# Kernel tuning notes

Measured on AMD Instinct MI355X. Metric: run time of the kernel, lower is better.

The kernel has to match this reference:

```python
import jax, jax.numpy as jnp
import numpy as np
import math

N_HEADS = 4
GELU = lambda x: jax.nn.gelu(x, approximate=False)  # torch nn.GELU default = exact erf

def _ln(x, s, b):
    m = jnp.mean(x, axis=-1, keepdims=True)
    v = jnp.mean((x - m) ** 2, axis=-1, keepdims=True)
    return (x - m) * jax.lax.rsqrt(v + 1e-5) * s + b

def _fwd(materials, in_seq, proj_vars, param_vars, enc_w1, enc_b1, enc_w2, enc_b2, sos,
         tl_wq, tl_wk, tl_wv, tl_bq, tl_bk, tl_bv, tl_wo, tl_bo,
         tl_ln1s, tl_ln1b, tl_ln2s, tl_ln2b, tl_fw1, tl_fb1, tl_fw2, tl_fb2,
         pw1, pb1, pw2, pb2, pw3, pb3, pw4, pb4, pw5, pb5,
         ipw1, ipb1, ipw2, ipb2, hw1, hb1, hw2, hb2, hw3, hb3):
    B = in_seq.shape[0]
    # encoder input MLP: [B,S,1] -> [B,S,D]
    x = GELU(in_seq @ enc_w1 + enc_b1) @ enc_w2 + enc_b2
    x = jnp.concatenate([jnp.broadcast_to(sos, (B, 1, sos.shape[-1])), x], axis=1)
    S1, D = x.shape[1], x.shape[2]
    dh = D // N_HEADS
    # sinusoidal positional encoding
    pos = jnp.arange(S1, dtype=jnp.float32)[:, None]
    div = jnp.exp(jnp.arange(0, D, 2, dtype=jnp.float32) * (-math.log(10000.0) / D))
    ang = pos * div
    pe = jnp.stack([jnp.sin(ang), jnp.cos(ang)], axis=-1).reshape(S1, D)
    x = x + pe
    scale = 1.0 / math.sqrt(dh)
    # post-LN TransformerEncoder layers (torch default norm_first=False), eval mode (no dropout)
    for l in range(tl_wq.shape[0]):
        q = (x @ tl_wq[l] + tl_bq[l]).reshape(B, S1, N_HEADS, dh).transpose(0, 2, 1, 3)
        k = (x @ tl_wk[l] + tl_bk[l]).reshape(B, S1, N_HEADS, dh).transpose(0, 2, 1, 3)
        v = (x @ tl_wv[l] + tl_bv[l]).reshape(B, S1, N_HEADS, dh).transpose(0, 2, 1, 3)
        att = jax.nn.softmax(jnp.einsum('bhqd,bhkd->bhqk', q, k) * scale, axis=-1)
        o = jnp.einsum('bhqk,bhkd->bhqd', att, v).transpose(0, 2, 1, 3).reshape(B, S1, D)
        x = _ln(x + o @ tl_wo[l] + tl_bo[l], tl_ln1s[l], tl_ln1b[l])
        f = GELU(x @ tl_fw1[l] + tl_fb1[l]) @ tl_fw2[l] + tl_fb2[l]
        x = _ln(x + f, tl_ln2s[l], tl_ln2b[l])
    sos_out = x[:, 0]
    h = jnp.concatenate([proj_vars, sos_out], axis=1)
    for w, b in ((pw1, pb1), (pw2, pb2), (pw3, pb3), (pw4, pb4)):
        h = GELU(h @ w + b)
    proj_out = h @ pw5 + pb5
    pp = GELU(param_vars @ ipw1 + ipb1) @ ipw2 + ipb2
    mi = jnp.concatenate([pp, proj_out], axis=1)  # [B, output_features+param_vars]
    # MaterialHead mask-gather-MLP-scatter == run every tiny head densely, pick by material id
    h1 = GELU(jnp.einsum('bi,mio->mbo', mi, hw1) + hb1[:, None, :])
    h2 = GELU(jnp.einsum('mbi,mio->mbo', h1, hw2) + hb2[:, None, :])
    h3 = jnp.einsum('mbi,mio->mbo', h2, hw3) + hb3[:, None, :]  # [M,B,1]
    return h3[materials, jnp.arange(B)]  # [B,1]

def setup_inputs() -> dict:
    key = jax.random.key(0)
    ks = iter(jax.random.split(key, 64))
    def rn(shape, scale=0.05):
        return jax.random.normal(next(ks), shape, dtype=jnp.float32) * scale
    B, S, IN, EL, D, L, DFF = 64, 1024, 1, 48, 64, 3, 256
    PV, PP, OF, M = 3, 3, 24, 3
    IF = OF + PP
    return dict(
        in_seq=rn((B, S, IN), 1.0),
        proj_vars=rn((B, PV), 1.0),
        param_vars=rn((B, PP), 1.0),
        materials=jax.random.randint(next(ks), (B,), 0, M),
        enc_w1=rn((IN, EL)), enc_b1=rn((EL,)), enc_w2=rn((EL, D)), enc_b2=rn((D,)),
        sos=rn((1, 1, D)),
        tl_wq=rn((L, D, D)), tl_wk=rn((L, D, D)), tl_wv=rn((L, D, D)),
        tl_bq=rn((L, D)), tl_bk=rn((L, D)), tl_bv=rn((L, D)),
        tl_wo=rn((L, D, D)), tl_bo=rn((L, D)),
        tl_ln1s=jnp.ones((L, D)), tl_ln1b=jnp.zeros((L, D)),
        tl_ln2s=jnp.ones((L, D)), tl_ln2b=jnp.zeros((L, D)),
        tl_fw1=rn((L, D, DFF)), tl_fb1=rn((L, DFF)), tl_fw2=rn((L, DFF, D)), tl_fb2=rn((L, D)),
        pw1=rn((PV + D, 34)), pb1=rn((34,)), pw2=rn((34, 11)), pb2=rn((11,)),
        pw3=rn((11, 36)), pb3=rn((36,)), pw4=rn((36, 22)), pb4=rn((22,)),
        pw5=rn((22, OF)), pb5=rn((OF,)),
        ipw1=rn((PP, 3)), ipb1=rn((3,)), ipw2=rn((3, PP)), ipb2=rn((PP,)),
        hw1=rn((M, IF, 15)), hb1=rn((M, 15)), hw2=rn((M, 15, 18)), hb2=rn((M, 18)),
        hw3=rn((M, 18, 1)), hb3=rn((M, 1)),
    )

def reference(in_seq, proj_vars, param_vars, materials, enc_w1, enc_b1, enc_w2, enc_b2, sos,
              tl_wq, tl_wk, tl_wv, tl_bq, tl_bk, tl_bv, tl_wo, tl_bo,
              tl_ln1s, tl_ln1b, tl_ln2s, tl_ln2b, tl_fw1, tl_fb1, tl_fw2, tl_fb2,
              pw1, pb1, pw2, pb2, pw3, pb3, pw4, pb4, pw5, pb5,
              ipw1, ipb1, ipw2, ipb2, hw1, hb1, hw2, hb2, hw3, hb3):
    return _fwd(materials, in_seq, proj_vars, param_vars, enc_w1, enc_b1, enc_w2, enc_b2, sos,
                tl_wq, tl_wk, tl_wv, tl_bq, tl_bk, tl_bv, tl_wo, tl_bo,
                tl_ln1s, tl_ln1b, tl_ln2s, tl_ln2b, tl_fw1, tl_fb1, tl_fw2, tl_fb2,
                pw1, pb1, pw2, pb2, pw3, pb3, pw4, pb4, pw5, pb5,
                ipw1, ipb1, ipw2, ipb2, hw1, hb1, hw2, hb2, hw3, hb3)
```

## Files before the change

kernel.cpp:

```cpp
#include <hip/hip_runtime.h>
#include <hip/hip_bf16.h>
#include <math.h>

#define BB   64
#define SS   1024
#define S1C  1025
#define DD   64
#define NHD  4
#define NBH  (BB * NHD)
#define DHD  16
#define DFFC 256
#define NLAY 3
#define NTOK (BB * S1C)
#define SPAD 1056
#define TGRP 11
#define FTQ   32
#define FT2   32
#define OPAD 68
#define QSCL 0.36067376022224085f

typedef const float* fp;
typedef __attribute__((ext_vector_type(8))) short bf16x8;
typedef __attribute__((ext_vector_type(4))) float f32x4;
typedef __attribute__((ext_vector_type(2))) unsigned int u32x2;
typedef __attribute__((ext_vector_type(4))) unsigned int u32x4;

#if __has_builtin(__builtin_amdgcn_exp2f)
#define RAW_EXP2(x) __builtin_amdgcn_exp2f(x)
#else
#define RAW_EXP2(x) __expf(0.6931471805599453f * (x))
#endif
#if __has_builtin(__builtin_amdgcn_rcpf)
#define RAW_RCP(x) __builtin_amdgcn_rcpf(x)
#else
#define RAW_RCP(x) (1.0f / (x))
#endif

__device__ __forceinline__ float gelu_exact(float x) {
    return 0.5f * x * (1.0f + erff(x * 0.7071067811865475f));
}
__device__ __forceinline__ float erf_fast(float x) {
    float ax = fabsf(x);
    float t = RAW_RCP(1.0f + 0.3275911f * ax);
    float p = t * (0.254829592f + t * (-0.284496736f + t * (1.421413741f +
              t * (-1.453152027f + t * 1.061405429f))));
    float e = RAW_EXP2(ax * ax * -1.4426950408889634f);
    float r = 1.0f - p * e;
    return copysignf(r, x);
}
__device__ __forceinline__ float gelu_fast(float x) {
    return 0.5f * x * (1.0f + erf_fast(x * 0.7071067811865475f));
}
__device__ __forceinline__ short f2b(float f) {
    unsigned u = __float_as_uint(f);
    return (short)((u + 0x7fffu + ((u >> 16) & 1u)) >> 16);
}

__device__ __forceinline__ u32x2 pack4exp(f32x4 c, bool valid) {
    float e0 = valid ? RAW_EXP2(c[0]) : 0.f;
    float e1 = valid ? RAW_EXP2(c[1]) : 0.f;
    float e2 = valid ? RAW_EXP2(c[2]) : 0.f;
    float e3 = valid ? RAW_EXP2(c[3]) : 0.f;
    unsigned r0, r1;
    asm("v_cvt_pk_bf16_f32 %0, %1, %2" : "=v"(r0) : "v"(e0), "v"(e1));
    asm("v_cvt_pk_bf16_f32 %0, %1, %2" : "=v"(r1) : "v"(e2), "v"(e3));
    return (u32x2){r0, r1};
}
__device__ __forceinline__ u32x2 pack4cvt(float x0, float x1, float x2, float x3) {
    unsigned r0, r1;
    asm("v_cvt_pk_bf16_f32 %0, %1, %2" : "=v"(r0) : "v"(x0), "v"(x1));
    asm("v_cvt_pk_bf16_f32 %0, %1, %2" : "=v"(r1) : "v"(x2), "v"(x3));
    return (u32x2){r0, r1};
}

__global__ __launch_bounds__(256) void k_wconv(
    fp wq, fp wk, fp wv, fp wo, fp w1, fp w2,
    short* __restrict__ wqkvT, short* __restrict__ woT,
    short* __restrict__ w1T, short* __restrict__ w2T)
{
    int l = blockIdx.y;
    int i = blockIdx.x * 256 + threadIdx.x;
    if (i < 12288) {
        int p = i >> 12, rem = i & 4095;
        int d = rem >> 6, j = rem & 63;
        fp src = (p == 0 ? wq : p == 1 ? wk : wv) + (size_t)l * 4096;
        float v = src[j * 64 + d];
        if (p == 0) v *= QSCL;
        wqkvT[(size_t)l * 12288 + i] = f2b(v);
    } else if (i < 16384) {
        int rem = i - 12288;
        woT[(size_t)l * 4096 + rem] = f2b(wo[(size_t)l * 4096 + (rem & 63) * 64 + (rem >> 6)]);
    } else if (i < 32768) {
        int rem = i - 16384;
        w1T[(size_t)l * 16384 + rem] = f2b(w1[(size_t)l * 16384 + (rem & 63) * 256 + (rem >> 6)]);
    } else {
        int rem = i - 32768;
        w2T[(size_t)l * 16384 + rem] = f2b(w2[(size_t)l * 16384 + (rem & 255) * 64 + (rem >> 8)]);
    }
}

__global__ __launch_bounds__(64) void k_zero(
    short* __restrict__ qb, short* __restrict__ kb, short* __restrict__ vbt)
{
    int bh = blockIdx.x, t = threadIdx.x;
    for (int i = t; i < 31 * 16; i += 64) {
        int r = i >> 4, c = i & 15;
        size_t idx = ((size_t)bh * SPAD + 1025 + r) * 16 + c;
        qb[idx] = 0; kb[idx] = 0;
    }
    for (int i = t; i < 16 * 31; i += 64) {
        int e = i / 31, c = i % 31;
        vbt[((size_t)bh * 16 + e) * SPAD + 1025 + c] = 0;
    }
}

__global__ __launch_bounds__(256) void k_encqkv(
    fp in_seq, fp enc_w1, fp enc_b1, fp enc_w2, fp enc_b2, fp sos,
    const short* __restrict__ wqkvT, fp bq, fp bk, fp bv,
    float* __restrict__ x,
    short* __restrict__ qb, short* __restrict__ kb, short* __restrict__ vbt)
{
    int t = threadIdx.x;
    int tok0 = blockIdx.x * FTQ;
    int w = t >> 6, d = t & 63;
    __shared__ float e[4][48];
    __shared__ short xs[FTQ][72];

    int i2 = (d >> 1) * 2;
    float factor = RAW_EXP2((float)i2 * (-9.210340371976184f / 64.0f) * 1.4426950408889634f);
    for (int i = 0; i < 8; ++i) {
        int tl = i * 4 + w;
        int tok = tok0 + tl;
        int b = tok / S1C, s = tok % S1C;
        float val;
        if (s == 0) {
            val = sos[d];
        } else {
            float tin = in_seq[b * SS + (s - 1)];
            if (d < 48) e[w][d] = gelu_fast(tin * enc_w1[d] + enc_b1[d]);
            float acc = enc_b2[d];
            for (int j = 0; j < 48; ++j) acc += e[w][j] * enc_w2[j * DD + d];
            val = acc;
        }
        float ang = (float)s * factor;
        val += (d & 1) ? __cosf(ang) : __sinf(ang);
        x[(size_t)tok * DD + d] = val;
        xs[tl][d] = f2b(val);
    }
    __syncthreads();

    int l = t & 63;
    int quad = l >> 4, lo = l & 15;
    bf16x8 a0 = *(const bf16x8*)&xs[lo][quad * 8];
    bf16x8 a1 = *(const bf16x8*)&xs[lo][32 + quad * 8];
    bf16x8 a2 = *(const bf16x8*)&xs[16 + lo][quad * 8];
    bf16x8 a3 = *(const bf16x8*)&xs[16 + lo][32 + quad * 8];

    int n = w * 16 + lo;
    #pragma unroll
    for (int p = 0; p < 3; ++p) {
        const short* wT = wqkvT + (size_t)p * 4096 + (size_t)n * 64;
        bf16x8 b0 = *(const bf16x8*)(wT + quad * 8);
        bf16x8 b1 = *(const bf16x8*)(wT + 32 + quad * 8);
        f32x4 c0 = __builtin_amdgcn_mfma_f32_16x16x32_bf16(a0, b0, (f32x4){0,0,0,0}, 0, 0, 0);
        c0 = __builtin_amdgcn_mfma_f32_16x16x32_bf16(a1, b1, c0, 0, 0, 0);
        f32x4 c1 = __builtin_amdgcn_mfma_f32_16x16x32_bf16(a2, b0, (f32x4){0,0,0,0}, 0, 0, 0);
        c1 = __builtin_amdgcn_mfma_f32_16x16x32_bf16(a3, b1, c1, 0, 0, 0);
        float bias = (p == 0) ? bq[n] * QSCL : (p == 1) ? bk[n] : bv[n];
        #pragma unroll
        for (int r = 0; r < 4; ++r) {
            int tok = tok0 + quad * 4 + r;
            int bb0 = tok / S1C, ss0 = tok % S1C;
            int bh = bb0 * NHD + w;
            short val = f2b(c0[r] + bias);
            int tok2 = tok + 16;
            int bb1 = tok2 / S1C, ss1 = tok2 % S1C;
            int bh2 = bb1 * NHD + w;
            short val2 = f2b(c1[r] + bias);
            if (p == 0) {
                qb[((size_t)bh * SPAD + ss0) * 16 + lo] = val;
                qb[((size_t)bh2 * SPAD + ss1) * 16 + lo] = val2;
            } else if (p == 1) {
                kb[((size_t)bh * SPAD + ss0) * 16 + lo] = val;
                kb[((size_t)bh2 * SPAD + ss1) * 16 + lo] = val2;
            } else {
                vbt[((size_t)bh * 16 + lo) * SPAD + ss0] = val;
                vbt[((size_t)bh2 * 16 + lo) * SPAD + ss1] = val2;
            }
        }
    }
}

__global__ __launch_bounds__(128) void k_attn(
    const short* __restrict__ qb, const short* __restrict__ kb,
    const short* __restrict__ vbt, short* __restrict__ ob)
{
    int bid = blockIdx.x;
    int bh  = bid % NBH;
    int grp = bid / NBH;
    int b = bh >> 2, h = bh & 3;
    int t = threadIdx.x;
    int w = t >> 6, l = t & 63;
    int quad = l >> 4, lo = l & 15;
    int t0 = grp * 2 + w;
    int t1 = t0 + 22;
    int t2 = t0 + 44;
    int qg0 = t0 * 16, qg1 = t1 * 16, qg2 = t2 * 16;

    __shared__ u32x2 ptmem[2][408];
    char* ptc = (char*)&ptmem[w][0];
    unsigned ptbase = (unsigned)(uintptr_t)ptc;

    const short* qbase = qb + (size_t)bh * SPAD * 16;
    const short* kbase = kb + (size_t)bh * SPAD * 16;
    const short* vbase = vbt + (size_t)bh * 16 * SPAD;

    bf16x8 aQ0 = {0,0,0,0,0,0,0,0}, aQ1 = {0,0,0,0,0,0,0,0}, aQ2 = {0,0,0,0,0,0,0,0};
    if (quad < 2) {
        aQ0 = *(const bf16x8*)(qbase + ((size_t)(qg0 + lo)) * 16 + quad * 8);
        aQ1 = *(const bf16x8*)(qbase + ((size_t)(qg1 + lo)) * 16 + quad * 8);
        aQ2 = *(const bf16x8*)(qbase + ((size_t)(qg2 + lo)) * 16 + quad * 8);
    }

    const short ONE = 0x3F80;
    bf16x8 aOne = {ONE, ONE, ONE, ONE, ONE, ONE, ONE, ONE};

    f32x4 oc0 = {0.f,0.f,0.f,0.f}, oc1 = {0.f,0.f,0.f,0.f}, oc2 = {0.f,0.f,0.f,0.f};
    f32x4 dn0 = {0.f,0.f,0.f,0.f}, dn1 = {0.f,0.f,0.f,0.f}, dn2 = {0.f,0.f,0.f,0.f};

    unsigned wo0 = (unsigned)((lo >> 2) * 136 + (lo & 3) * 32 + quad * 8);
    unsigned ro = (unsigned)(quad * 272 + lo * 8);
    unsigned rdp = ptbase + ro;
    char* wbp = ptc + wo0;

    bf16x8 kxA, kyA, kxB, kyB, vA, vB;

    {
        const short* k0p = kbase + (size_t)lo * 16 + (quad & 1) * 8;
        kxA = *(const bf16x8*)k0p;
        kyA = *(const bf16x8*)(k0p + 256);
        vA  = *(const bf16x8*)(vbase + (size_t)lo * SPAD + quad * 8);
        const short* k1p = kbase + (size_t)(32 + lo) * 16 + (quad & 1) * 8;
        kxB = *(const bf16x8*)k1p;
        kyB = *(const bf16x8*)(k1p + 256);

        f32x4 c0 = __builtin_amdgcn_mfma_f32_16x16x32_bf16(aQ0, kxA, (f32x4){0.f,0.f,0.f,0.f}, 0, 0, 0);
        f32x4 c1 = __builtin_amdgcn_mfma_f32_16x16x32_bf16(aQ1, kxA, (f32x4){0.f,0.f,0.f,0.f}, 0, 0, 0);
        f32x4 c2 = __builtin_amdgcn_mfma_f32_16x16x32_bf16(aQ2, kxA, (f32x4){0.f,0.f,0.f,0.f}, 0, 0, 0);
        *(u32x2*)(wbp)        = pack4exp(c0, true);
        *(u32x2*)(wbp + 1088) = pack4exp(c1, true);
        *(u32x2*)(wbp + 2176) = pack4exp(c2, true);
        c0 = __builtin_amdgcn_mfma_f32_16x16x32_bf16(aQ0, kyA, (f32x4){0.f,0.f,0.f,0.f}, 0, 0, 0);
        c1 = __builtin_amdgcn_mfma_f32_16x16x32_bf16(aQ1, kyA, (f32x4){0.f,0.f,0.f,0.f}, 0, 0, 0);
        c2 = __builtin_amdgcn_mfma_f32_16x16x32_bf16(aQ2, kyA, (f32x4){0.f,0.f,0.f,0.f}, 0, 0, 0);
        *(u32x2*)(wbp + 544)  = pack4exp(c0, true);
        *(u32x2*)(wbp + 1632) = pack4exp(c1, true);
        *(u32x2*)(wbp + 2720) = pack4exp(c2, true);
    }

#define STEP(CH, TAIL, KXC, KYC, KXN, KYN, VP, VC) do {                       \
    int ch_ = (CH);                                                            \
    if (!(TAIL)) {                                                             \
        const short* kn_ = kbase + (size_t)((ch_ + 1) * 32 + lo) * 16 + (quad & 1) * 8; \
        KXN = *(const bf16x8*)kn_;                                             \
        KYN = *(const bf16x8*)(kn_ + 256);                                     \
    }                                                                          \
    VC = *(const bf16x8*)(vbase + (size_t)lo * SPAD + ch_ * 32 + quad * 8);    \
    u32x2 p00_, p01_, p10_, p11_, p20_, p21_;                                  \
    asm volatile("ds_read_b64_tr_b16 %0, %1"             : "=v"(p00_) : "v"(rdp) : "memory"); \
    asm volatile("ds_read_b64_tr_b16 %0, %1 offset:136"  : "=v"(p01_) : "v"(rdp) : "memory"); \
    asm volatile("ds_read_b64_tr_b16 %0, %1 offset:1088" : "=v"(p10_) : "v"(rdp) : "memory"); \
    asm volatile("ds_read_b64_tr_b16 %0, %1 offset:1224" : "=v"(p11_) : "v"(rdp) : "memory"); \
    asm volatile("ds_read_b64_tr_b16 %0, %1 offset:2176" : "=v"(p20_) : "v"(rdp) : "memory"); \
    asm volatile("ds_read_b64_tr_b16 %0, %1 offset:2312" : "=v"(p21_) : "v"(rdp) : "memory"); \
    u32x2 wt0x_, wt1x_, wt2x_, wt0y_, wt1y_, wt2y_;                            \
    {                                                                          \
        f32x4 c0_ = __builtin_amdgcn_mfma_f32_16x16x32_bf16(aQ0, KXC, (f32x4){0.f,0.f,0.f,0.f}, 0, 0, 0); \
        f32x4 c1_ = __builtin_amdgcn_mfma_f32_16x16x32_bf16(aQ1, KXC, (f32x4){0.f,0.f,0.f,0.f}, 0, 0, 0); \
        f32x4 c2_ = __builtin_amdgcn_mfma_f32_16x16x32_bf16(aQ2, KXC, (f32x4){0.f,0.f,0.f,0.f}, 0, 0, 0); \
        bool v0_ = !(TAIL) || (lo == 0);                                       \
        wt0x_ = pack4exp(c0_, v0_);                                            \
        wt1x_ = pack4exp(c1_, v0_);                                            \
        wt2x_ = pack4exp(c2_, v0_);                                            \
        c0_ = __builtin_amdgcn_mfma_f32_16x16x32_bf16(aQ0, KYC, (f32x4){0.f,0.f,0.f,0.f}, 0, 0, 0); \
        c1_ = __builtin_amdgcn_mfma_f32_16x16x32_bf16(aQ1, KYC, (f32x4){0.f,0.f,0.f,0.f}, 0, 0, 0); \
        c2_ = __builtin_amdgcn_mfma_f32_16x16x32_bf16(aQ2, KYC, (f32x4){0.f,0.f,0.f,0.f}, 0, 0, 0); \
        bool v1_ = !(TAIL);                                                    \
        wt0y_ = pack4exp(c0_, v1_);                                            \
        wt1y_ = pack4exp(c1_, v1_);                                            \
        wt2y_ = pack4exp(c2_, v1_);                                            \
    }                                                                          \
    asm volatile("s_waitcnt lgkmcnt(0)" ::: "memory");                         \
    __builtin_amdgcn_sched_barrier(0);                                         \
    u32x4 q0_; q0_[0] = p00_[0]; q0_[1] = p00_[1]; q0_[2] = p01_[0]; q0_[3] = p01_[1]; \
    u32x4 q1_; q1_[0] = p10_[0]; q1_[1] = p10_[1]; q1_[2] = p11_[0]; q1_[3] = p11_[1]; \
    u32x4 q2_; q2_[0] = p20_[0]; q2_[1] = p20_[1]; q2_[2] = p21_[0]; q2_[3] = p21_[1]; \
    bf16x8 pB0_ = __builtin_bit_cast(bf16x8, q0_);                             \
    bf16x8 pB1_ = __builtin_bit_cast(bf16x8, q1_);                             \
    bf16x8 pB2_ = __builtin_bit_cast(bf16x8, q2_);                             \
    oc0 = __builtin_amdgcn_mfma_f32_16x16x32_bf16(VP, pB0_, oc0, 0, 0, 0);     \
    dn0 = __builtin_amdgcn_mfma_f32_16x16x32_bf16(aOne, pB0_, dn0, 0, 0, 0);   \
    oc1 = __builtin_amdgcn_mfma_f32_16x16x32_bf16(VP, pB1_, oc1, 0, 0, 0);     \
    dn1 = __builtin_amdgcn_mfma_f32_16x16x32_bf16(aOne, pB1_, dn1, 0, 0, 0);   \
    oc2 = __builtin_amdgcn_mfma_f32_16x16x32_bf16(VP, pB2_, oc2, 0, 0, 0);     \
    dn2 = __builtin_amdgcn_mfma_f32_16x16x32_bf16(aOne, pB2_, dn2, 0, 0, 0);   \
    *(u32x2*)(wbp)        = wt0x_;                                             \
    *(u32x2*)(wbp + 544)  = wt0y_;                                             \
    *(u32x2*)(wbp + 1088) = wt1x_;                                             \
    *(u32x2*)(wbp + 1632) = wt1y_;                                             \
    *(u32x2*)(wbp + 2176) = wt2x_;                                             \
    *(u32x2*)(wbp + 2720) = wt2y_;                                             \
} while (0)

    for (int chp = 1; chp < 31; chp += 2) {
        STEP(chp,     0, kxA, kyA, kxB, kyB, vA, vB);
        STEP(chp + 1, 0, kxB, kyB, kxA, kyA, vB, vA);
    }
    STEP(31, 0, kxA, kyA, kxB, kyB, vA, vB);
    STEP(32, 1, kxB, kyB, kxA, kyA, vB, vA);
#undef STEP

    {
        u32x2 p00, p01, p10, p11, p20, p21;
        asm volatile("ds_read_b64_tr_b16 %0, %1"             : "=v"(p00) : "v"(rdp) : "memory");
        asm volatile("ds_read_b64_tr_b16 %0, %1 offset:136"  : "=v"(p01) : "v"(rdp) : "memory");
        asm volatile("ds_read_b64_tr_b16 %0, %1 offset:1088" : "=v"(p10) : "v"(rdp) : "memory");
        asm volatile("ds_read_b64_tr_b16 %0, %1 offset:1224" : "=v"(p11) : "v"(rdp) : "memory");
        asm volatile("ds_read_b64_tr_b16 %0, %1 offset:2176" : "=v"(p20) : "v"(rdp) : "memory");
        asm volatile("ds_read_b64_tr_b16 %0, %1 offset:2312" : "=v"(p21) : "v"(rdp) : "memory");
        asm volatile("s_waitcnt lgkmcnt(0)" ::: "memory");
        __builtin_amdgcn_sched_barrier(0);
        u32x4 q0; q0[0] = p00[0]; q0[1] = p00[1]; q0[2] = p01[0]; q0[3] = p01[1];
        u32x4 q1; q1[0] = p10[0]; q1[1] = p10[1]; q1[2] = p11[0]; q1[3] = p11[1];
        u32x4 q2; q2[0] = p20[0]; q2[1] = p20[1]; q2[2] = p21[0]; q2[3] = p21[1];
        bf16x8 pB0 = __builtin_bit_cast(bf16x8, q0);
        bf16x8 pB1 = __builtin_bit_cast(bf16x8, q1);
        bf16x8 pB2 = __builtin_bit_cast(bf16x8, q2);
        oc0 = __builtin_amdgcn_mfma_f32_16x16x32_bf16(vA, pB0, oc0, 0, 0, 0);
        dn0 = __builtin_amdgcn_mfma_f32_16x16x32_bf16(aOne, pB0, dn0, 0, 0, 0);
        oc1 = __builtin_amdgcn_mfma_f32_16x16x32_bf16(vA, pB1, oc1, 0, 0, 0);
        dn1 = __builtin_amdgcn_mfma_f32_16x16x32_bf16(aOne, pB1, dn1, 0, 0, 0);
        oc2 = __builtin_amdgcn_mfma_f32_16x16x32_bf16(vA, pB2, oc2, 0, 0, 0);
        dn2 = __builtin_amdgcn_mfma_f32_16x16x32_bf16(aOne, pB2, dn2, 0, 0, 0);
    }

    {
        int qrow = qg0 + lo;
        if (qrow < S1C) {
            float inv = 1.0f / dn0[0];
            unsigned p0 = (unsigned short)f2b(oc0[0] * inv) | ((unsigned)(unsigned short)f2b(oc0[1] * inv) << 16);
            unsigned p1 = (unsigned short)f2b(oc0[2] * inv) | ((unsigned)(unsigned short)f2b(oc0[3] * inv) << 16);
            *(uint2*)(ob + ((size_t)b * S1C + qrow) * DD + h * DHD + quad * 4) = make_uint2(p0, p1);
        }
    }
    {
        int qrow = qg1 + lo;
        if (qrow < S1C) {
            float inv = 1.0f / dn1[0];
            unsigned p0 = (unsigned short)f2b(oc1[0] * inv) | ((unsigned)(unsigned short)f2b(oc1[1] * inv) << 16);
            unsigned p1 = (unsigned short)f2b(oc1[2] * inv) | ((unsigned)(unsigned short)f2b(oc1[3] * inv) << 16);
            *(uint2*)(ob + ((size_t)b * S1C + qrow) * DD + h * DHD + quad * 4) = make_uint2(p0, p1);
        }
    }
    {
        int qrow = qg2 + lo;
        if (qrow < S1C) {
            float inv = 1.0f / dn2[0];
            unsigned p0 = (unsigned short)f2b(oc2[0] * inv) | ((unsigned)(unsigned short)f2b(oc2[1] * inv) << 16);
            unsigned p1 = (unsigned short)f2b(oc2[2] * inv) | ((unsigned)(unsigned short)f2b(oc2[3] * inv) << 16);
            *(uint2*)(ob + ((size_t)b * S1C + qrow) * DD + h * DHD + quad * 4) = make_uint2(p0, p1);
        }
    }
}

__global__ __launch_bounds__(256) void k_block(
    const short* __restrict__ ob, float* __restrict__ x,
    const short* __restrict__ woT, fp bo, fp ln1s, fp ln1b,
    const short* __restrict__ w1T, fp b1, const short* __restrict__ w2T, fp b2,
    fp ln2s, fp ln2b,
    const short* __restrict__ wqkvTn, fp bqn, fp bkn, fp bvn,
    short* __restrict__ qb, short* __restrict__ kb, short* __restrict__ vbt,
    int has_next)
{
    int blk = blockIdx.x, t = threadIdx.x;
    int tok0 = blk * FT2;
    int w = t >> 6, l = t & 63;
    int quad = l >> 4, lo = l & 15;

    __shared__ float otf[FT2][OPAD];
    __shared__ u32x2 hidtr[2][8][136];
    short* ysb = (short*)&otf[0][0];
    char*  hidc = (char*)&hidtr[0][0][0];
    unsigned hidbase = (unsigned)(uintptr_t)hidc;

    int tt8 = t >> 3;
    int d8s = (t & 7) * 8;
    const float* xrow = x + (size_t)(tok0 + tt8) * DD + d8s;
    float4 xpa = *(const float4*)xrow;
    float4 xpb = *(const float4*)(xrow + 4);
    float4 s1a = *(const float4*)(ln1s + d8s);
    float4 s1b = *(const float4*)(ln1s + d8s + 4);
    float4 b1a = *(const float4*)(ln1b + d8s);
    float4 b1b = *(const float4*)(ln1b + d8s + 4);

    {
        const short* obp0 = ob + ((size_t)(tok0 + lo)) * DD;
        const short* obp1 = ob + ((size_t)(tok0 + 16 + lo)) * DD;
        bf16x8 a0 = *(const bf16x8*)(obp0 + quad * 8);
        bf16x8 a1 = *(const bf16x8*)(obp0 + 32 + quad * 8);
        bf16x8 a2 = *(const bf16x8*)(obp1 + quad * 8);
        bf16x8 a3 = *(const bf16x8*)(obp1 + 32 + quad * 8);
        int n = w * 16 + lo;
        const short* wT = woT + (size_t)n * 64;
        bf16x8 b0 = *(const bf16x8*)(wT + quad * 8);
        bf16x8 bb = *(const bf16x8*)(wT + 32 + quad * 8);
        f32x4 c0 = __builtin_amdgcn_mfma_f32_16x16x32_bf16(a0, b0, (f32x4){0,0,0,0}, 0, 0, 0);
        c0 = __builtin_amdgcn_mfma_f32_16x16x32_bf16(a1, bb, c0, 0, 0, 0);
        f32x4 c1 = __builtin_amdgcn_mfma_f32_16x16x32_bf16(a2, b0, (f32x4){0,0,0,0}, 0, 0, 0);
        c1 = __builtin_amdgcn_mfma_f32_16x16x32_bf16(a3, bb, c1, 0, 0, 0);
        float bov = bo[n];
        #pragma unroll
        for (int r = 0; r < 4; ++r) {
            otf[quad * 4 + r][n] = c0[r] + bov;
            otf[16 + quad * 4 + r][n] = c1[r] + bov;
        }
    }
    __syncthreads();

    float yv[8];
    {
        float4 o0 = *(const float4*)&otf[tt8][d8s];
        float4 o1 = *(const float4*)&otf[tt8][d8s + 4];
        float v0 = o0.x + xpa.x, v1 = o0.y + xpa.y, v2 = o0.z + xpa.z, v3 = o0.w + xpa.w;
        float v4 = o1.x + xpb.x, v5 = o1.y + xpb.y, v6 = o1.z + xpb.z, v7 = o1.w + xpb.w;
        float sum = ((v0 + v1) + (v2 + v3)) + ((v4 + v5) + (v6 + v7));
        float vs = v0 * v0;
        vs = fmaf(v1, v1, vs); vs = fmaf(v2, v2, vs); vs = fmaf(v3, v3, vs);
        vs = fmaf(v4, v4, vs); vs = fmaf(v5, v5, vs); vs = fmaf(v6, v6, vs);
        vs = fmaf(v7, v7, vs);
        sum += __shfl_xor(sum, 1, 64); sum += __shfl_xor(sum, 2, 64); sum += __shfl_xor(sum, 4, 64);
        vs  += __shfl_xor(vs , 1, 64); vs  += __shfl_xor(vs , 2, 64); vs  += __shfl_xor(vs , 4, 64);
        float mean = sum * (1.0f / 64.0f);
        float var = vs * (1.0f / 64.0f) - mean * mean;
        float rs = rsqrtf(var + 1e-5f);
        yv[0] = (v0 - mean) * rs * s1a.x + b1a.x;
        yv[1] = (v1 - mean) * rs * s1a.y + b1a.y;
        yv[2] = (v2 - mean) * rs * s1a.z + b1a.z;
        yv[3] = (v3 - mean) * rs * s1a.w + b1a.w;
        yv[4] = (v4 - mean) * rs * s1b.x + b1b.x;
        yv[5] = (v5 - mean) * rs * s1b.y + b1b.y;
        yv[6] = (v6 - mean) * rs * s1b.z + b1b.z;
        yv[7] = (v7 - mean) * rs * s1b.w + b1b.w;
        u32x2 pa = pack4cvt(yv[0], yv[1], yv[2], yv[3]);
        u32x2 pb = pack4cvt(yv[4], yv[5], yv[6], yv[7]);
        *(u32x4*)&ysb[tt8 * 136 + d8s] = (u32x4){pa[0], pa[1], pb[0], pb[1]};
    }
    __syncthreads();

    {
        bf16x8 a0 = *(const bf16x8*)&ysb[(size_t)lo * 136 + quad * 8];
        bf16x8 a1 = *(const bf16x8*)&ysb[(size_t)lo * 136 + 32 + quad * 8];
        bf16x8 a2 = *(const bf16x8*)&ysb[(size_t)(16 + lo) * 136 + quad * 8];
        bf16x8 a3 = *(const bf16x8*)&ysb[(size_t)(16 + lo) * 136 + 32 + quad * 8];
        unsigned hoff = (unsigned)(w * 2176 + (lo >> 2) * 136 + (lo & 3) * 32 + quad * 8);
        #pragma unroll
        for (int i = 0; i < 4; ++i) {
            int n = w * 64 + i * 16 + lo;
            const short* wT = w1T + (size_t)n * 64;
            bf16x8 b0 = *(const bf16x8*)(wT + quad * 8);
            bf16x8 bb = *(const bf16x8*)(wT + 32 + quad * 8);
            f32x4 c0 = __builtin_amdgcn_mfma_f32_16x16x32_bf16(a0, b0, (f32x4){0,0,0,0}, 0, 0, 0);
            c0 = __builtin_amdgcn_mfma_f32_16x16x32_bf16(a1, bb, c0, 0, 0, 0);
            f32x4 c1 = __builtin_amdgcn_mfma_f32_16x16x32_bf16(a2, b0, (f32x4){0,0,0,0}, 0, 0, 0);
            c1 = __builtin_amdgcn_mfma_f32_16x16x32_bf16(a3, bb, c1, 0, 0, 0);
            float b1v = b1[n];
            unsigned off = hoff + (i >> 1) * 1088 + (i & 1) * 544;
            *(u32x2*)(hidc + off) = pack4cvt(
                gelu_fast(c0[0] + b1v), gelu_fast(c0[1] + b1v),
                gelu_fast(c0[2] + b1v), gelu_fast(c0[3] + b1v));
            *(u32x2*)(hidc + 8704 + off) = pack4cvt(
                gelu_fast(c1[0] + b1v), gelu_fast(c1[1] + b1v),
                gelu_fast(c1[2] + b1v), gelu_fast(c1[3] + b1v));
        }
    }
    __syncthreads();

    {
        f32x4 c20 = {0.f,0.f,0.f,0.f}, c21 = {0.f,0.f,0.f,0.f};
        const short* wT2 = w2T + (size_t)(w * 16 + lo) * 256;
        unsigned ro = (unsigned)(quad * 272 + lo * 8);
        unsigned tb0 = hidbase + ro;
        unsigned tb1 = hidbase + 8704 + ro;
        u32x2 pA0, pA1, pA2, pA3, pB0, pB1, pB2, pB3;

#define TRRD(dst, addr, OFFSTR) \
    asm volatile("ds_read_b64_tr_b16 %0, %1 offset:" OFFSTR : "=v"(dst) : "v"(addr))
#define ISS(P0,P1,P2,P3, O1, O2) \
    TRRD(P0, tb0, O1); TRRD(P1, tb0, O2); TRRD(P2, tb1, O1); TRRD(P3, tb1, O2)
#define W4 asm volatile("s_waitcnt lgkmcnt(4)" ::: "memory"); __builtin_amdgcn_sched_barrier(0)
#define W0 asm volatile("s_waitcnt lgkmcnt(0)" ::: "memory"); __builtin_amdgcn_sched_barrier(0)
#define CONS(P0,P1,P2,P3, BF) do { \
    u32x4 q0_; q0_[0]=P0[0]; q0_[1]=P0[1]; q0_[2]=P1[0]; q0_[3]=P1[1]; \
    u32x4 q1_; q1_[0]=P2[0]; q1_[1]=P2[1]; q1_[2]=P3[0]; q1_[3]=P3[1]; \
    c20 = __builtin_amdgcn_mfma_f32_16x16x32_bf16(__builtin_bit_cast(bf16x8,q0_), BF, c20, 0,0,0); \
    c21 = __builtin_amdgcn_mfma_f32_16x16x32_bf16(__builtin_bit_cast(bf16x8,q1_), BF, c21, 0,0,0); \
} while (0)

        bf16x8 bfA = *(const bf16x8*)(wT2 + quad * 8);
        ISS(pA0,pA1,pA2,pA3, "0",    "136");
        bf16x8 bfB = *(const bf16x8*)(wT2 + 32 + quad * 8);
        ISS(pB0,pB1,pB2,pB3, "1088", "1224");
        W4; CONS(pA0,pA1,pA2,pA3, bfA);
        bfA = *(const bf16x8*)(wT2 + 64 + quad * 8);
        ISS(pA0,pA1,pA2,pA3, "2176", "2312");
        W4; CONS(pB0,pB1,pB2,pB3, bfB);
        bfB = *(const bf16x8*)(wT2 + 96 + quad * 8);
        ISS(pB0,pB1,pB2,pB3, "3264", "3400");
        W4; CONS(pA0,pA1,pA2,pA3, bfA);
        bfA = *(const bf16x8*)(wT2 + 128 + quad * 8);
        ISS(pA0,pA1,pA2,pA3, "4352", "4488");
        W4; CONS(pB0,pB1,pB2,pB3, bfB);
        bfB = *(const bf16x8*)(wT2 + 160 + quad * 8);
        ISS(pB0,pB1,pB2,pB3, "5440", "5576");
        W4; CONS(pA0,pA1,pA2,pA3, bfA);
        bfA = *(const bf16x8*)(wT2 + 192 + quad * 8);
        ISS(pA0,pA1,pA2,pA3, "6528", "6664");
        W4; CONS(pB0,pB1,pB2,pB3, bfB);
        bfB = *(const bf16x8*)(wT2 + 224 + quad * 8);
        ISS(pB0,pB1,pB2,pB3, "7616", "7752");
        W4; CONS(pA0,pA1,pA2,pA3, bfA);
        W0; CONS(pB0,pB1,pB2,pB3, bfB);
#undef TRRD
#undef ISS
#undef W4
#undef W0
#undef CONS

        float b2v = b2[w * 16 + lo];
        #pragma unroll
        for (int r = 0; r < 4; ++r) {
            otf[quad * 4 + r][w * 16 + lo] = c20[r] + b2v;
            otf[16 + quad * 4 + r][w * 16 + lo] = c21[r] + b2v;
        }
    }
    __syncthreads();

    {
        float4 s2a = *(const float4*)(ln2s + d8s);
        float4 s2b = *(const float4*)(ln2s + d8s + 4);
        float4 b2a = *(const float4*)(ln2b + d8s);
        float4 b2b = *(const float4*)(ln2b + d8s + 4);
        float4 o0 = *(const float4*)&otf[tt8][d8s];
        float4 o1 = *(const float4*)&otf[tt8][d8s + 4];
        float v0 = o0.x + yv[0], v1 = o0.y + yv[1], v2 = o0.z + yv[2], v3 = o0.w + yv[3];
        float v4 = o1.x + yv[4], v5 = o1.y + yv[5], v6 = o1.z + yv[6], v7 = o1.w + yv[7];
        float sum = ((v0 + v1) + (v2 + v3)) + ((v4 + v5) + (v6 + v7));
        float vs = v0 * v0;
        vs = fmaf(v1, v1, vs); vs = fmaf(v2, v2, vs); vs = fmaf(v3, v3, vs);
        vs = fmaf(v4, v4, vs); vs = fmaf(v5, v5, vs); vs = fmaf(v6, v6, vs);
        vs = fmaf(v7, v7, vs);
        sum += __shfl_xor(sum, 1, 64); sum += __shfl_xor(sum, 2, 64); sum += __shfl_xor(sum, 4, 64);
        vs  += __shfl_xor(vs , 1, 64); vs  += __shfl_xor(vs , 2, 64); vs  += __shfl_xor(vs , 4, 64);
        float mean = sum * (1.0f / 64.0f);
        float var = vs * (1.0f / 64.0f) - mean * mean;
        float rs = rsqrtf(var + 1e-5f);
        float y0 = (v0 - mean) * rs * s2a.x + b2a.x;
        float y1 = (v1 - mean) * rs * s2a.y + b2a.y;
        float y2 = (v2 - mean) * rs * s2a.z + b2a.z;
        float y3 = (v3 - mean) * rs * s2a.w + b2a.w;
        float y4 = (v4 - mean) * rs * s2b.x + b2b.x;
        float y5 = (v5 - mean) * rs * s2b.y + b2b.y;
        float y6 = (v6 - mean) * rs * s2b.z + b2b.z;
        float y7 = (v7 - mean) * rs * s2b.w + b2b.w;
        float* xo = x + (size_t)(tok0 + tt8) * DD + d8s;
        *(float4*)xo = make_float4(y0, y1, y2, y3);
        *(float4*)(xo + 4) = make_float4(y4, y5, y6, y7);
        u32x2 pa = pack4cvt(y0, y1, y2, y3);
        u32x2 pb = pack4cvt(y4, y5, y6, y7);
        *(u32x4*)&ysb[tt8 * 136 + d8s] = (u32x4){pa[0], pa[1], pb[0], pb[1]};
    }
    __syncthreads();

    if (has_next) {
        bf16x8 a0 = *(const bf16x8*)&ysb[(size_t)lo * 136 + quad * 8];
        bf16x8 a1 = *(const bf16x8*)&ysb[(size_t)lo * 136 + 32 + quad * 8];
        bf16x8 a2 = *(const bf16x8*)&ysb[(size_t)(16 + lo) * 136 + quad * 8];
        bf16x8 a3 = *(const bf16x8*)&ysb[(size_t)(16 + lo) * 136 + 32 + quad * 8];
        int n = w * 16 + lo;
        #pragma unroll
        for (int p = 0; p < 3; ++p) {
            const short* wT = wqkvTn + (size_t)p * 4096 + (size_t)n * 64;
            bf16x8 b0 = *(const bf16x8*)(wT + quad * 8);
            bf16x8 bb = *(const bf16x8*)(wT + 32 + quad * 8);
            f32x4 c0 = __builtin_amdgcn_mfma_f32_16x16x32_bf16(a0, b0, (f32x4){0,0,0,0}, 0, 0, 0);
            c0 = __builtin_amdgcn_mfma_f32_16x16x32_bf16(a1, bb, c0, 0, 0, 0);
            f32x4 c1 = __builtin_amdgcn_mfma_f32_16x16x32_bf16(a2, b0, (f32x4){0,0,0,0}, 0, 0, 0);
            c1 = __builtin_amdgcn_mfma_f32_16x16x32_bf16(a3, bb, c1, 0, 0, 0);
            float bias = (p == 0) ? bqn[n] * QSCL : (p == 1) ? bkn[n] : bvn[n];
            #pragma unroll
            for (int r = 0; r < 4; ++r) {
                int tok = tok0 + quad * 4 + r;
                int bb0 = tok / S1C, ss0 = tok % S1C;
                int bh = bb0 * NHD + w;
                short val = f2b(c0[r] + bias);
                int tok2 = tok + 16;
                int bb1 = tok2 / S1C, ss1 = tok2 % S1C;
                int bh2 = bb1 * NHD + w;
                short val2 = f2b(c1[r] + bias);
                if (p == 0) {
                    qb[((size_t)bh * SPAD + ss0) * 16 + lo] = val;
                    qb[((size_t)bh2 * SPAD + ss1) * 16 + lo] = val2;
                } else if (p == 1) {
                    kb[((size_t)bh * SPAD + ss0) * 16 + lo] = val;
                    kb[((size_t)bh2 * SPAD + ss1) * 16 + lo] = val2;
                } else {
                    vbt[((size_t)bh * 16 + lo) * SPAD + ss0] = val;
                    vbt[((size_t)bh2 * 16 + lo) * SPAD + ss1] = val2;
                }
            }
        }
    }
}

__global__ __launch_bounds__(64) void k_head(
    const float* __restrict__ x, fp proj_vars, fp param_vars,
    const int* __restrict__ materials,
    fp pw1, fp pb1, fp pw2, fp pb2, fp pw3, fp pb3,
    fp pw4, fp pb4, fp pw5, fp pb5,
    fp ipw1, fp ipb1, fp ipw2, fp ipb2,
    fp hw1, fp hb1, fp hw2, fp hb2, fp hw3, fp hb3,
    float* __restrict__ out)
{
    int b = blockIdx.x;
    int tid = threadIdx.x;
    __shared__ float A[80], Bf[80], pp[8], mi[32];

    if (tid < 3) A[tid] = proj_vars[b * 3 + tid];
    A[3 + tid] = x[((size_t)b * S1C + 0) * DD + tid];
    __syncthreads();

    if (tid < 34) {
        float a = pb1[tid];
        for (int i = 0; i < 67; ++i) a += A[i] * pw1[i * 34 + tid];
        Bf[tid] = gelu_exact(a);
    }
    __syncthreads();
    if (tid < 11) {
        float a = pb2[tid];
        for (int i = 0; i < 34; ++i) a += Bf[i] * pw2[i * 11 + tid];
        A[tid] = gelu_exact(a);
    }
    __syncthreads();
    if (tid < 36) {
        float a = pb3[tid];
        for (int i = 0; i < 11; ++i) a += A[i] * pw3[i * 36 + tid];
        Bf[tid] = gelu_exact(a);
    }
    __syncthreads();
    if (tid < 22) {
        float a = pb4[tid];
        for (int i = 0; i < 36; ++i) a += Bf[i] * pw4[i * 22 + tid];
        A[tid] = gelu_exact(a);
    }
    __syncthreads();
    if (tid < 24) {
        float a = pb5[tid];
        for (int i = 0; i < 22; ++i) a += A[i] * pw5[i * 24 + tid];
        mi[3 + tid] = a;
    }
    if (tid < 3) {
        float a = ipb1[tid];
        for (int i = 0; i < 3; ++i) a += param_vars[b * 3 + i] * ipw1[i * 3 + tid];
        pp[tid] = gelu_exact(a);
    }
    __syncthreads();
    if (tid < 3) {
        float a = ipb2[tid];
        for (int i = 0; i < 3; ++i) a += pp[i] * ipw2[i * 3 + tid];
        mi[tid] = a;
    }
    __syncthreads();

    int m = materials[b];
    if (tid < 15) {
        float a = hb1[m * 15 + tid];
        for (int i = 0; i < 27; ++i) a += mi[i] * hw1[(m * 27 + i) * 15 + tid];
        A[tid] = gelu_exact(a);
    }
    __syncthreads();
    if (tid < 18) {
        float a = hb2[m * 18 + tid];
        for (int i = 0; i < 15; ++i) a += A[i] * hw2[(m * 15 + i) * 18 + tid];
        Bf[tid] = gelu_exact(a);
    }
    __syncthreads();
    if (tid == 0) {
        float a = hb3[m];
        for (int i = 0; i < 18; ++i) a += Bf[i] * hw3[m * 18 + i];
        out[b] = a;
    }
}

extern "C" void kernel_launch(void* const* d_in, const int* in_sizes, int n_in,
                              void* d_out, int out_size, void* d_ws, size_t ws_size,
                              hipStream_t stream) {
    fp in_seq     = (fp)d_in[0];
    fp proj_vars  = (fp)d_in[1];
    fp param_vars = (fp)d_in[2];
    const int* materials = (const int*)d_in[3];
    fp enc_w1 = (fp)d_in[4];
    fp enc_b1 = (fp)d_in[5];
    fp enc_w2 = (fp)d_in[6];
    fp enc_b2 = (fp)d_in[7];
    fp sos    = (fp)d_in[8];
    fp tl_wq  = (fp)d_in[9];
    fp tl_wk  = (fp)d_in[10];
    fp tl_wv  = (fp)d_in[11];
    fp tl_bq  = (fp)d_in[12];
    fp tl_bk  = (fp)d_in[13];
    fp tl_bv  = (fp)d_in[14];
    fp tl_wo  = (fp)d_in[15];
    fp tl_bo  = (fp)d_in[16];
    fp tl_ln1s = (fp)d_in[17];
    fp tl_ln1b = (fp)d_in[18];
    fp tl_ln2s = (fp)d_in[19];
    fp tl_ln2b = (fp)d_in[20];
    fp tl_fw1 = (fp)d_in[21];
    fp tl_fb1 = (fp)d_in[22];
    fp tl_fw2 = (fp)d_in[23];
    fp tl_fb2 = (fp)d_in[24];
    fp pw1 = (fp)d_in[25]; fp pb1 = (fp)d_in[26];
    fp pw2 = (fp)d_in[27]; fp pb2 = (fp)d_in[28];
    fp pw3 = (fp)d_in[29]; fp pb3 = (fp)d_in[30];
    fp pw4 = (fp)d_in[31]; fp pb4 = (fp)d_in[32];
    fp pw5 = (fp)d_in[33]; fp pb5 = (fp)d_in[34];
    fp ipw1 = (fp)d_in[35]; fp ipb1 = (fp)d_in[36];
    fp ipw2 = (fp)d_in[37]; fp ipb2 = (fp)d_in[38];
    fp hw1 = (fp)d_in[39]; fp hb1 = (fp)d_in[40];
    fp hw2 = (fp)d_in[41]; fp hb2 = (fp)d_in[42];
    fp hw3 = (fp)d_in[43]; fp hb3 = (fp)d_in[44];

    float* x  = (float*)d_ws;
    short* ob = (short*)(x + (size_t)NTOK * DD);
    short* xb = ob + (size_t)NTOK * DD;
    short* qb = xb + (size_t)NTOK * DD;
    short* kb = qb + (size_t)NBH * SPAD * 16;
    short* vbt = kb + (size_t)NBH * SPAD * 16;
    short* wqkvT = vbt + (size_t)NBH * 16 * SPAD;
    short* woT = wqkvT + (size_t)NLAY * 12288;
    short* w1T = woT + (size_t)NLAY * 4096;
    short* w2T = w1T + (size_t)NLAY * 16384;

    k_wconv<<<dim3(192, NLAY), 256, 0, stream>>>(
        tl_wq, tl_wk, tl_wv, tl_wo, tl_fw1, tl_fw2, wqkvT, woT, w1T, w2T);
    k_zero<<<NBH, 64, 0, stream>>>(qb, kb, vbt);
    k_encqkv<<<NTOK / FTQ, 256, 0, stream>>>(
        in_seq, enc_w1, enc_b1, enc_w2, enc_b2, sos,
        wqkvT, tl_bq, tl_bk, tl_bv,
        x, qb, kb, vbt);

    for (int l = 0; l < NLAY; ++l) {
        k_attn<<<NBH * TGRP, 128, 0, stream>>>(qb, kb, vbt, ob);
        int ln = (l + 1 < NLAY) ? (l + 1) : l;
        k_block<<<NTOK / FT2, 256, 0, stream>>>(
            ob, x,
            woT + (size_t)l * 4096, tl_bo + (size_t)l * DD,
            tl_ln1s + (size_t)l * DD, tl_ln1b + (size_t)l * DD,
            w1T + (size_t)l * 16384, tl_fb1 + (size_t)l * DFFC,
            w2T + (size_t)l * 16384, tl_fb2 + (size_t)l * DD,
            tl_ln2s + (size_t)l * DD, tl_ln2b + (size_t)l * DD,
            wqkvT + (size_t)ln * 12288,
            tl_bq + (size_t)ln * DD, tl_bk + (size_t)ln * DD, tl_bv + (size_t)ln * DD,
            qb, kb, vbt,
            (l + 1 < NLAY) ? 1 : 0);
    }

    k_head<<<BB, 64, 0, stream>>>(
        x, proj_vars, param_vars, materials,
        pw1, pb1, pw2, pb2, pw3, pb3, pw4, pb4, pw5, pb5,
        ipw1, ipb1, ipw2, ipb2,
        hw1, hb1, hw2, hb2, hw3, hb3,
        (float*)d_out);
}
```

Baseline: 471.0 us.

## Split attention key range across two waves per query tile and merge partials

The attention kernel now launches 256 threads per block. Each pair of waves shares the same query tiles and splits the key chunks in half, so each wave does about half the sequential chunk loop. Partial numerators and denominators go through shared memory, are summed after a block barrier, and one wave writes the output. This shortens the per-wave serial chain and raises wave count, at the cost of more shared memory, an extra sync, and a merge step.

```diff
diff --git a/kernel.cpp b/kernel.cpp
--- a/kernel.cpp
+++ b/kernel.cpp
@@ -191,7 +191,7 @@
     }
 }
 
-__global__ __launch_bounds__(128) void k_attn(
+__global__ __launch_bounds__(256) void k_attn(
     const short* __restrict__ qb, const short* __restrict__ kb,
     const short* __restrict__ vbt, short* __restrict__ ob)
 {
@@ -201,13 +201,14 @@
     int b = bh >> 2, h = bh & 3;
     int t = threadIdx.x;
     int w = t >> 6, l = t & 63;
+    int slot = w >> 1, half = w & 1;
     int quad = l >> 4, lo = l & 15;
-    int t0 = grp * 2 + w;
+    int t0 = grp * 2 + slot;
     int t1 = t0 + 22;
     int t2 = t0 + 44;
     int qg0 = t0 * 16, qg1 = t1 * 16, qg2 = t2 * 16;
 
-    __shared__ u32x2 ptmem[2][408];
+    __shared__ u32x2 ptmem[4][544];
     char* ptc = (char*)&ptmem[w][0];
     unsigned ptbase = (unsigned)(uintptr_t)ptc;
 
@@ -234,28 +235,29 @@
     char* wbp = ptc + wo0;
 
     bf16x8 kxA, kyA, kxB, kyB, vA, vB;
+    int c0 = half << 4;
 
     {
-        const short* k0p = kbase + (size_t)lo * 16 + (quad & 1) * 8;
+        const short* k0p = kbase + (size_t)(c0 * 32 + lo) * 16 + (quad & 1) * 8;
         kxA = *(const bf16x8*)k0p;
         kyA = *(const bf16x8*)(k0p + 256);
-        vA  = *(const bf16x8*)(vbase + (size_t)lo * SPAD + quad * 8);
-        const short* k1p = kbase + (size_t)(32 + lo) * 16 + (quad & 1) * 8;
+        vA  = *(const bf16x8*)(vbase + (size_t)lo * SPAD + c0 * 32 + quad * 8);
+        const short* k1p = kbase + (size_t)((c0 + 1) * 32 + lo) * 16 + (quad & 1) * 8;
         kxB = *(const bf16x8*)k1p;
         kyB = *(const bf16x8*)(k1p + 256);
 
-        f32x4 c0 = __builtin_amdgcn_mfma_f32_16x16x32_bf16(aQ0, kxA, (f32x4){0.f,0.f,0.f,0.f}, 0, 0, 0);
-        f32x4 c1 = __builtin_amdgcn_mfma_f32_16x16x32_bf16(aQ1, kxA, (f32x4){0.f,0.f,0.f,0.f}, 0, 0, 0);
-        f32x4 c2 = __builtin_amdgcn_mfma_f32_16x16x32_bf16(aQ2, kxA, (f32x4){0.f,0.f,0.f,0.f}, 0, 0, 0);
-        *(u32x2*)(wbp)        = pack4exp(c0, true);
-        *(u32x2*)(wbp + 1088) = pack4exp(c1, true);
-        *(u32x2*)(wbp + 2176) = pack4exp(c2, true);
-        c0 = __builtin_amdgcn_mfma_f32_16x16x32_bf16(aQ0, kyA, (f32x4){0.f,0.f,0.f,0.f}, 0, 0, 0);
-        c1 = __builtin_amdgcn_mfma_f32_16x16x32_bf16(aQ1, kyA, (f32x4){0.f,0.f,0.f,0.f}, 0, 0, 0);
-        c2 = __builtin_amdgcn_mfma_f32_16x16x32_bf16(aQ2, kyA, (f32x4){0.f,0.f,0.f,0.f}, 0, 0, 0);
-        *(u32x2*)(wbp + 544)  = pack4exp(c0, true);
-        *(u32x2*)(wbp + 1632) = pack4exp(c1, true);
-        *(u32x2*)(wbp + 2720) = pack4exp(c2, true);
+        f32x4 c0_ = __builtin_amdgcn_mfma_f32_16x16x32_bf16(aQ0, kxA, (f32x4){0.f,0.f,0.f,0.f}, 0, 0, 0);
+        f32x4 c1_ = __builtin_amdgcn_mfma_f32_16x16x32_bf16(aQ1, kxA, (f32x4){0.f,0.f,0.f,0.f}, 0, 0, 0);
+        f32x4 c2_ = __builtin_amdgcn_mfma_f32_16x16x32_bf16(aQ2, kxA, (f32x4){0.f,0.f,0.f,0.f}, 0, 0, 0);
+        *(u32x2*)(wbp)        = pack4exp(c0_, true);
+        *(u32x2*)(wbp + 1088) = pack4exp(c1_, true);
+        *(u32x2*)(wbp + 2176) = pack4exp(c2_, true);
+        c0_ = __builtin_amdgcn_mfma_f32_16x16x32_bf16(aQ0, kyA, (f32x4){0.f,0.f,0.f,0.f}, 0, 0, 0);
+        c1_ = __builtin_amdgcn_mfma_f32_16x16x32_bf16(aQ1, kyA, (f32x4){0.f,0.f,0.f,0.f}, 0, 0, 0);
+        c2_ = __builtin_amdgcn_mfma_f32_16x16x32_bf16(aQ2, kyA, (f32x4){0.f,0.f,0.f,0.f}, 0, 0, 0);
+        *(u32x2*)(wbp + 544)  = pack4exp(c0_, true);
+        *(u32x2*)(wbp + 1632) = pack4exp(c1_, true);
+        *(u32x2*)(wbp + 2720) = pack4exp(c2_, true);
     }
 
 #define STEP(CH, TAIL, KXC, KYC, KXN, KYN, VP, VC) do {                       \
@@ -312,63 +314,96 @@
     *(u32x2*)(wbp + 2720) = wt2y_;                                             \
 } while (0)
 
-    for (int chp = 1; chp < 31; chp += 2) {
-        STEP(chp,     0, kxA, kyA, kxB, kyB, vA, vB);
-        STEP(chp + 1, 0, kxB, kyB, kxA, kyA, vB, vA);
-    }
-    STEP(31, 0, kxA, kyA, kxB, kyB, vA, vB);
-    STEP(32, 1, kxB, kyB, kxA, kyA, vB, vA);
+#define EPILOGUE(VLAST) do {                                                   \
+    u32x2 p00, p01, p10, p11, p20, p21;                                        \
+    asm volatile("ds_read_b64_tr_b16 %0, %1"             : "=v"(p00) : "v"(rdp) : "memory"); \
+    asm volatile("ds_read_b64_tr_b16 %0, %1 offset:136"  : "=v"(p01) : "v"(rdp) : "memory"); \
+    asm volatile("ds_read_b64_tr_b16 %0, %1 offset:1088" : "=v"(p10) : "v"(rdp) : "memory"); \
+    asm volatile("ds_read_b64_tr_b16 %0, %1 offset:1224" : "=v"(p11) : "v"(rdp) : "memory"); \
+    asm volatile("ds_read_b64_tr_b16 %0, %1 offset:2176" : "=v"(p20) : "v"(rdp) : "memory"); \
+    asm volatile("ds_read_b64_tr_b16 %0, %1 offset:2312" : "=v"(p21) : "v"(rdp) : "memory"); \
+    asm volatile("s_waitcnt lgkmcnt(0)" ::: "memory");                         \
+    __builtin_amdgcn_sched_barrier(0);                                         \
+    u32x4 q0; q0[0] = p00[0]; q0[1] = p00[1]; q0[2] = p01[0]; q0[3] = p01[1];  \
+    u32x4 q1; q1[0] = p10[0]; q1[1] = p10[1]; q1[2] = p11[0]; q1[3] = p11[1];  \
+    u32x4 q2; q2[0] = p20[0]; q2[1] = p20[1]; q2[2] = p21[0]; q2[3] = p21[1];  \
+    bf16x8 pB0 = __builtin_bit_cast(bf16x8, q0);                               \
+    bf16x8 pB1 = __builtin_bit_cast(bf16x8, q1);                               \
+    bf16x8 pB2 = __builtin_bit_cast(bf16x8, q2);                               \
+    oc0 = __builtin_amdgcn_mfma_f32_16x16x32_bf16(VLAST, pB0, oc0, 0, 0, 0);   \
+    dn0 = __builtin_amdgcn_mfma_f32_16x16x32_bf16(aOne, pB0, dn0, 0, 0, 0);    \
+    oc1 = __builtin_amdgcn_mfma_f32_16x16x32_bf16(VLAST, pB1, oc1, 0, 0, 0);   \
+    dn1 = __builtin_amdgcn_mfma_f32_16x16x32_bf16(aOne, pB1, dn1, 0, 0, 0);    \
+    oc2 = __builtin_amdgcn_mfma_f32_16x16x32_bf16(VLAST, pB2, oc2, 0, 0, 0);   \
+    dn2 = __builtin_amdgcn_mfma_f32_16x16x32_bf16(aOne, pB2, dn2, 0, 0, 0);    \
+} while (0)
+
+    if (half == 0) {
+        for (int ch = 1; ch < 15; ch += 2) {
+            STEP(ch,     0, kxB, kyB, kxA, kyA, vA, vB);
+            STEP(ch + 1, 0, kxA, kyA, kxB, kyB, vB, vA);
+        }
+        STEP(15, 0, kxB, kyB, kxA, kyA, vA, vB);
+        EPILOGUE(vB);
+    } else {
+        for (int ch = 17; ch < 31; ch += 2) {
+            STEP(ch,     0, kxB, kyB, kxA, kyA, vA, vB);
+            STEP(ch + 1, 0, kxA, kyA, kxB, kyB, vB, vA);
+        }
+        STEP(31, 0, kxB, kyB, kxA, kyA, vA, vB);
+        STEP(32, 1, kxA, kyA, kxB, kyB, vB, vA);
+        EPILOGUE(vA);
+    }
 #undef STEP
+#undef EPILOGUE
 
     {
-        u32x2 p00, p01, p10, p11, p20, p21;
-        asm volatile("ds_read_b64_tr_b16 %0, %1"             : "=v"(p00) : "v"(rdp) : "memory");
-        asm volatile("ds_read_b64_tr_b16 %0, %1 offset:136"  : "=v"(p01) : "v"(rdp) : "memory");
-        asm volatile("ds_read_b64_tr_b16 %0, %1 offset:1088" : "=v"(p10) : "v"(rdp) : "memory");
-        asm volatile("ds_read_b64_tr_b16 %0, %1 offset:1224" : "=v"(p11) : "v"(rdp) : "memory");
-        asm volatile("ds_read_b64_tr_b16 %0, %1 offset:2176" : "=v"(p20) : "v"(rdp) : "memory");
-        asm volatile("ds_read_b64_tr_b16 %0, %1 offset:2312" : "=v"(p21) : "v"(rdp) : "memory");
-        asm volatile("s_waitcnt lgkmcnt(0)" ::: "memory");
-        __builtin_amdgcn_sched_barrier(0);
-        u32x4 q0; q0[0] = p00[0]; q0[1] = p00[1]; q0[2] = p01[0]; q0[3] = p01[1];
-        u32x4 q1; q1[0] = p10[0]; q1[1] = p10[1]; q1[2] = p11[0]; q1[3] = p11[1];
-        u32x4 q2; q2[0] = p20[0]; q2[1] = p20[1]; q2[2] = p21[0]; q2[3] = p21[1];
-        bf16x8 pB0 = __builtin_bit_cast(bf16x8, q0);
-        bf16x8 pB1 = __builtin_bit_cast(bf16x8, q1);
-        bf16x8 pB2 = __builtin_bit_cast(bf16x8, q2);
-        oc0 = __builtin_amdgcn_mfma_f32_16x16x32_bf16(vA, pB0, oc0, 0, 0, 0);
-        dn0 = __builtin_amdgcn_mfma_f32_16x16x32_bf16(aOne, pB0, dn0, 0, 0, 0);
-        oc1 = __builtin_amdgcn_mfma_f32_16x16x32_bf16(vA, pB1, oc1, 0, 0, 0);
-        dn1 = __builtin_amdgcn_mfma_f32_16x16x32_bf16(aOne, pB1, dn1, 0, 0, 0);
-        oc2 = __builtin_amdgcn_mfma_f32_16x16x32_bf16(vA, pB2, oc2, 0, 0, 0);
-        dn2 = __builtin_amdgcn_mfma_f32_16x16x32_bf16(aOne, pB2, dn2, 0, 0, 0);
-    }
-
-    {
-        int qrow = qg0 + lo;
-        if (qrow < S1C) {
-            float inv = 1.0f / dn0[0];
-            unsigned p0 = (unsigned short)f2b(oc0[0] * inv) | ((unsigned)(unsigned short)f2b(oc0[1] * inv) << 16);
-            unsigned p1 = (unsigned short)f2b(oc0[2] * inv) | ((unsigned)(unsigned short)f2b(oc0[3] * inv) << 16);
-            *(uint2*)(ob + ((size_t)b * S1C + qrow) * DD + h * DHD + quad * 4) = make_uint2(p0, p1);
-        }
-    }
-    {
-        int qrow = qg1 + lo;
-        if (qrow < S1C) {
-            float inv = 1.0f / dn1[0];
-            unsigned p0 = (unsigned short)f2b(oc1[0] * inv) | ((unsigned)(unsigned short)f2b(oc1[1] * inv) << 16);
-            unsigned p1 = (unsigned short)f2b(oc1[2] * inv) | ((unsigned)(unsigned short)f2b(oc1[3] * inv) << 16);
-            *(uint2*)(ob + ((size_t)b * S1C + qrow) * DD + h * DHD + quad * 4) = make_uint2(p0, p1);
-        }
-    }
-    {
-        int qrow = qg2 + lo;
-        if (qrow < S1C) {
-            float inv = 1.0f / dn2[0];
-            unsigned p0 = (unsigned short)f2b(oc2[0] * inv) | ((unsigned)(unsigned short)f2b(oc2[1] * inv) << 16);
-            unsigned p1 = (unsigned short)f2b(oc2[2] * inv) | ((unsigned)(unsigned short)f2b(oc2[3] * inv) << 16);
-            *(uint2*)(ob + ((size_t)b * S1C + qrow) * DD + h * DHD + quad * 4) = make_uint2(p0, p1);
+        float* pb = (float*)ptc;
+        int base = l * 17;
+        pb[base + 0] = oc0[0]; pb[base + 1] = oc0[1];
+        pb[base + 2] = oc0[2]; pb[base + 3] = oc0[3]; pb[base + 4] = dn0[0];
+        pb[base + 5] = oc1[0]; pb[base + 6] = oc1[1];
+        pb[base + 7] = oc1[2]; pb[base + 8] = oc1[3]; pb[base + 9] = dn1[0];
+        pb[base +10] = oc2[0]; pb[base +11] = oc2[1];
+        pb[base +12] = oc2[2]; pb[base +13] = oc2[3]; pb[base +14] = dn2[0];
+    }
+    __syncthreads();
+
+    if (half == 0) {
+        const float* pp = (const float*)&ptmem[w ^ 1][0];
+        int base = l * 17;
+        {
+            int qrow = qg0 + lo;
+            if (qrow < S1C) {
+                float inv = 1.0f / (dn0[0] + pp[base + 4]);
+                float s0 = oc0[0] + pp[base + 0], s1 = oc0[1] + pp[base + 1];
+                float s2 = oc0[2] + pp[base + 2], s3 = oc0[3] + pp[base + 3];
+                unsigned p0 = (unsigned short)f2b(s0 * inv) | ((unsigned)(unsigned short)f2b(s1 * inv) << 16);
+                unsigned p1 = (unsigned short)f2b(s2 * inv) | ((unsigned)(unsigned short)f2b(s3 * inv) << 16);
+                *(uint2*)(ob + ((size_t)b * S1C + qrow) * DD + h * DHD + quad * 4) = make_uint2(p0, p1);
+            }
+        }
+        {
+            int qrow = qg1 + lo;
+            if (qrow < S1C) {
+                float inv = 1.0f / (dn1[0] + pp[base + 9]);
+                float s0 = oc1[0] + pp[base + 5], s1 = oc1[1] + pp[base + 6];
+                float s2 = oc1[2] + pp[base + 7], s3 = oc1[3] + pp[base + 8];
+                unsigned p0 = (unsigned short)f2b(s0 * inv) | ((unsigned)(unsigned short)f2b(s1 * inv) << 16);
+                unsigned p1 = (unsigned short)f2b(s2 * inv) | ((unsigned)(unsigned short)f2b(s3 * inv) << 16);
+                *(uint2*)(ob + ((size_t)b * S1C + qrow) * DD + h * DHD + quad * 4) = make_uint2(p0, p1);
+            }
+        }
+        {
+            int qrow = qg2 + lo;
+            if (qrow < S1C) {
+                float inv = 1.0f / (dn2[0] + pp[base + 14]);
+                float s0 = oc2[0] + pp[base + 10], s1 = oc2[1] + pp[base + 11];
+                float s2 = oc2[2] + pp[base + 12], s3 = oc2[3] + pp[base + 13];
+                unsigned p0 = (unsigned short)f2b(s0 * inv) | ((unsigned)(unsigned short)f2b(s1 * inv) << 16);
+                unsigned p1 = (unsigned short)f2b(s2 * inv) | ((unsigned)(unsigned short)f2b(s3 * inv) << 16);
+                *(uint2*)(ob + ((size_t)b * S1C + qrow) * DD + h * DHD + quad * 4) = make_uint2(p0, p1);
+            }
         }
     }
 }
@@ -760,7 +795,7 @@
         x, qb, kb, vbt);
 
     for (int l = 0; l < NLAY; ++l) {
-        k_attn<<<NBH * TGRP, 128, 0, stream>>>(qb, kb, vbt, ob);
+        k_attn<<<NBH * TGRP, 256, 0, stream>>>(qb, kb, vbt, ob);
         int ln = (l + 1 < NLAY) ? (l + 1) : l;
         k_block<<<NTOK / FT2, 256, 0, stream>>>(
             ob, x,
```

Result: no change. 463.2 us (-1.7%).
